# Optimization experiments

Measured on AMD Instinct MI355X. Metric: run time of the kernel, lower is better.

## Reference

```python
import jax, jax.numpy as jnp
import numpy as np

# ---- geometry constants (LinearProbeGeom) ----
N_DET, N_T = 128, 2048
NX, NY = 128, 256
PITCH, DT = 3.0e-4, 2.5e-8
C_SOUND = 1540.0
X0, DX = 0.0, 3.0e-4
Y0, DY = 1.0e-3, 1.5e-4
ARRAY_X0, ARRAY_Y = 0.0, 0.0

_freq = np.fft.rfftfreq(N_T, d=DT).astype(np.float32)
OMEGA = jnp.asarray(2.0 * np.pi * _freq, dtype=jnp.float32)            # [n_f]
KX = jnp.asarray((2.0 * np.pi * np.fft.fftfreq(N_DET, d=PITCH)).astype(np.float32))  # [n_det]
_fw = np.ones(_freq.shape[0], dtype=np.float32)
if _fw.shape[0] > 2:
    _fw[1:-1] = 2.0
if N_T % 2 == 0 and _fw.shape[0] > 1:
    _fw[-1] = 1.0
FREQ_W = jnp.asarray(_fw)                                              # [n_f]
XC = jnp.asarray((X0 + np.arange(NX) * DX - ARRAY_X0).astype(np.float32))  # [nx]
YC = jnp.asarray((Y0 + np.arange(NY) * DY - ARRAY_Y).astype(np.float32))   # [ny]


def setup_inputs() -> dict:
    key = jax.random.key(0)
    sino = jax.random.normal(key, (8, 2, N_DET, N_T), dtype=jnp.float32)
    # Hann window apodization (non-trainable buffer in the torch module)
    win = 0.5 - 0.5 * np.cos(2 * np.pi * np.arange(N_DET) / max(N_DET - 1, 1))
    apod = jnp.asarray(win.astype(np.float32))
    return {"sino": sino, "apod": apod}


def reference(sino, apod):
    B, C, n_det, n_t = sino.shape
    eps = jnp.finfo(jnp.float32).eps
    # per-(B,C) standardization over (n_det, n_t)
    mean = sino.mean(axis=(-2, -1), keepdims=True)
    sn = sino - mean
    std = jnp.sqrt(jnp.mean(sn * sn, axis=(-2, -1), keepdims=True) + eps)
    sn = sn / std
    sw = sn * apod[None, None, :, None]
    # temporal rFFT then spatial FFT over detectors -> [B,C,n_det,n_f] complex64
    spec = jnp.fft.fft(jnp.fft.rfft(sw, axis=-1), axis=2)
    kz_sq = (OMEGA / C_SOUND)[None, :] ** 2 - (KX ** 2)[:, None]       # [n_det,n_f]
    kz = jnp.sqrt(jnp.clip(kz_sq, 0.0))
    spec = spec * (kz_sq > 0).astype(spec.dtype)
    # phase factors (vectorized over all ny depths -> one big contraction)
    phase_x = jnp.exp(1j * KX[:, None] * XC[None, :]).astype(spec.dtype)        # [n_det,nx]
    phase_y = jnp.exp(1j * YC[:, None, None] * kz[None, :, :]).astype(spec.dtype)  # [ny,n_det,n_f]
    specw = spec * FREQ_W.astype(spec.dtype)[None, None, None, :]
    band = jnp.einsum('bcdf,ydf->bcyd', specw, phase_y)                # sum over freq
    img_c = jnp.einsum('bcyd,dx->bcyx', band, phase_x)                 # [B,C,ny,nx]
    img = jnp.abs(img_c).astype(sino.dtype)
    norm = jnp.maximum(apod.sum(), eps) * jnp.maximum(FREQ_W.sum(), eps)
    return img / norm
```

## Files before the change

### kernel.cpp

```cpp
#include <hip/hip_runtime.h>
#include <math.h>

#define N_DETC 128
#define N_TC   2048
#define N_FC   1025
#define N_FP   1056
#define NXC    128
#define NYC    256
#define NBCC   16

#define MPAD(i) ((i) + ((i) >> 5))

typedef short bf16x8 __attribute__((ext_vector_type(8)));
typedef float f32x4  __attribute__((ext_vector_type(4)));

__device__ __forceinline__ float2 cmulf(float2 a, float2 b){
    return make_float2(a.x*b.x - a.y*b.y, a.x*b.y + a.y*b.x);
}

#if __has_builtin(__builtin_amdgcn_sinf) && __has_builtin(__builtin_amdgcn_cosf)
__device__ __forceinline__ float sin_rev(float tf){ return __builtin_amdgcn_sinf(tf); }
__device__ __forceinline__ float cos_rev(float tf){ return __builtin_amdgcn_cosf(tf); }
#else
__device__ __forceinline__ float sin_rev(float tf){ return __sinf(6.28318530718f * tf); }
__device__ __forceinline__ float cos_rev(float tf){ return __cosf(6.28318530718f * tf); }
#endif

__device__ __forceinline__ ushort cvt_bf16(float x){
    uint u = __float_as_uint(x);
    return (ushort)((u + 0x7FFFu + ((u >> 16) & 1u)) >> 16);
}

__global__ __launch_bounds__(256) void k_tfft(const float* __restrict__ sino,
                                              float* __restrict__ psum,
                                              float* __restrict__ psq,
                                              uint* __restrict__ spec_u){
    int row = blockIdx.x;
    __shared__ float2 z[1055];
    __shared__ float ls[4], lq[4];
    int tid = threadIdx.x;
    const float2* p = (const float2*)(sino + (size_t)row * N_TC);
    float s = 0.f, q = 0.f;
    for (int n = tid; n < 1024; n += 256){
        float2 v = p[n];
        s += v.x + v.y;
        q += v.x * v.x + v.y * v.y;
        int r = __brev((unsigned)n) >> 22;
        z[MPAD(r)] = v;
    }
    #pragma unroll
    for (int m = 1; m < 64; m <<= 1){
        s += __shfl_xor(s, m, 64);
        q += __shfl_xor(q, m, 64);
    }
    int w = tid >> 6, lane = tid & 63;
    if (lane == 0){ ls[w] = s; lq[w] = q; }
    __syncthreads();
    if (tid == 0){
        psum[row] = ls[0] + ls[1] + ls[2] + ls[3];
        psq[row]  = lq[0] + lq[1] + lq[2] + lq[3];
    }
    #pragma unroll
    for (int st = 0; st < 5; ++st){
        int h = 1 << (2 * st);
        int qd = tid;
        int k = qd & (h - 1);
        int g = qd >> (2 * st);
        int base = (g << (2 * st + 2)) + k;
        float2 x0 = z[MPAD(base)];
        float2 x1 = z[MPAD(base + h)];
        float2 x2 = z[MPAD(base + 2 * h)];
        float2 x3 = z[MPAD(base + 3 * h)];
        float a1 = -(float)M_PI * (float)k / (float)h;
        float s1, c1; __sincosf(a1, &s1, &c1);
        float a2 = 0.5f * a1;
        float s2, c2; __sincosf(a2, &s2, &c2);
        float2 t1 = make_float2(x1.x * c1 - x1.y * s1, x1.x * s1 + x1.y * c1);
        float2 t3 = make_float2(x3.x * c1 - x3.y * s1, x3.x * s1 + x3.y * c1);
        float2 y0 = make_float2(x0.x + t1.x, x0.y + t1.y);
        float2 y1 = make_float2(x0.x - t1.x, x0.y - t1.y);
        float2 y2 = make_float2(x2.x + t3.x, x2.y + t3.y);
        float2 y3 = make_float2(x2.x - t3.x, x2.y - t3.y);
        float2 u = make_float2(y2.x * c2 - y2.y * s2, y2.x * s2 + y2.y * c2);
        float2 v = make_float2(y3.x * c2 - y3.y * s2, y3.x * s2 + y3.y * c2);
        float2 wv = make_float2(v.y, -v.x);
        z[MPAD(base)]         = make_float2(y0.x + u.x, y0.y + u.y);
        z[MPAD(base + 2 * h)] = make_float2(y0.x - u.x, y0.y - u.y);
        z[MPAD(base + h)]     = make_float2(y1.x + wv.x, y1.y + wv.y);
        z[MPAD(base + 3 * h)] = make_float2(y1.x - wv.x, y1.y - wv.y);
        __syncthreads();
    }
    uint* o = spec_u + (size_t)row * N_FC;
    for (int k = tid; k < 1025; k += 256){
        float2 A  = z[MPAD(k & 1023)];
        float2 Bv = z[MPAD((1024 - k) & 1023)];
        float Br = Bv.x, Bi = -Bv.y;
        float Er = 0.5f * (A.x + Br), Ei = 0.5f * (A.y + Bi);
        float Dr = 0.5f * (A.x - Br), Di = 0.5f * (A.y - Bi);
        float Or = Di, Oi = -Dr;
        float ang = -(float)M_PI * (float)k * (1.0f / 1024.0f);
        float sn, cs; __sincosf(ang, &sn, &cs);
        float Xr = Er + cs * Or - sn * Oi;
        float Xi = Ei + cs * Oi + sn * Or;
        uint pk;
        asm("v_cvt_pk_bf16_f32 %0, %1, %2" : "=v"(pk) : "v"(Xr), "v"(Xi));
        o[k] = pk;
    }
}

__global__ __launch_bounds__(256) void k_dft(const uint* __restrict__ spec_u,
                                             const float* __restrict__ psum,
                                             const float* __restrict__ psq,
                                             const float* __restrict__ apod,
                                             ushort* __restrict__ Arp,
                                             ushort* __restrict__ Aip,
                                             float4* __restrict__ kzJ){
    int bid = blockIdx.x;
    int ft = bid >> 4, bc = bid & 15;
    int f0 = ft << 5;
    int tid = threadIdx.x;
    __shared__ float2 tile[128][33];
    __shared__ ushort stAr[128][40];
    __shared__ ushort stAi[128][40];
    __shared__ float sm[2];

    if (tid < 64){
        float s = psum[bc * 128 + tid] + psum[bc * 128 + 64 + tid];
        float q = psq[bc * 128 + tid] + psq[bc * 128 + 64 + tid];
        #pragma unroll
        for (int m = 1; m < 64; m <<= 1){
            s += __shfl_xor(s, m, 64);
            q += __shfl_xor(q, m, 64);
        }
        if (tid == 0){
            const float inv_n = 1.f / (float)(N_DETC * N_TC);
            float mean = s * inv_n;
            float var  = q * inv_n - mean * mean;
            sm[0] = mean;
            sm[1] = rsqrtf(fmaxf(var, 0.f) + 1.1920929e-7f);
        }
    }
    __syncthreads();
    float mean = sm[0], invstd = sm[1];

    int fl  = tid & 31;
    int kd0 = tid >> 5;
    int f = f0 + fl;
    bool fok = (f <= 1024);
    float fr = (float)f * 19531.25f;
    float oc = fr * (1.0f / 1540.0f);

    #pragma unroll
    for (int i = 0; i < 16; ++i){
        int kd = kd0 + (i << 3);
        int rkd = __brev((unsigned)kd) >> 25;
        uint u = fok ? spec_u[((size_t)(bc * 128 + kd)) * N_FC + f] : 0u;
        float vr = __uint_as_float(u << 16);
        float vi = __uint_as_float(u & 0xFFFF0000u);
        if (f == 0) vr -= mean * 2048.f;
        float sc = apod[kd] * invstd;
        tile[rkd][fl] = make_float2(vr * sc, vi * sc);
    }
    if (bc == 0){
        #pragma unroll
        for (int i = 0; i < 16; ++i){
            int kd = kd0 + (i << 3);
            int sdx = (kd < 64) ? kd : kd - 128;
            float bb = (float)sdx * 26.0416666f;
            float kq = oc * oc - bb * bb;
            float kzr = (fok && kq > 0.f) ? sqrtf(kq) : 0.f;
            float tj = 1.5e-4f * kzr;
            tj -= floorf(tj);
            kzJ[(size_t)kd * N_FP + f] = make_float4(kzr, cos_rev(tj), sin_rev(tj), 0.f);
        }
    }
    __syncthreads();
    #pragma unroll
    for (int st = 0; st < 3; ++st){
        int h = 1 << (2 * st);
        #pragma unroll
        for (int it = 0; it < 4; ++it){
            int task = tid + (it << 8);
            int ff = task & 31;
            int q  = task >> 5;
            int k = q & (h - 1);
            int g = q >> (2 * st);
            int base = (g << (2 * st + 2)) + k;
            float2 x0 = tile[base][ff];
            float2 x1 = tile[base + h][ff];
            float2 x2 = tile[base + 2 * h][ff];
            float2 x3 = tile[base + 3 * h][ff];
            float a1 = -(float)M_PI * (float)k / (float)h;
            float s1, c1; __sincosf(a1, &s1, &c1);
            float a2 = 0.5f * a1;
            float s2, c2; __sincosf(a2, &s2, &c2);
            float2 t1 = make_float2(x1.x * c1 - x1.y * s1, x1.x * s1 + x1.y * c1);
            float2 t3 = make_float2(x3.x * c1 - x3.y * s1, x3.x * s1 + x3.y * c1);
            float2 y0 = make_float2(x0.x + t1.x, x0.y + t1.y);
            float2 y1 = make_float2(x0.x - t1.x, x0.y - t1.y);
            float2 y2 = make_float2(x2.x + t3.x, x2.y + t3.y);
            float2 y3 = make_float2(x2.x - t3.x, x2.y - t3.y);
            float2 u = make_float2(y2.x * c2 - y2.y * s2, y2.x * s2 + y2.y * c2);
            float2 v = make_float2(y3.x * c2 - y3.y * s2, y3.x * s2 + y3.y * c2);
            float2 w = make_float2(v.y, -v.x);
            tile[base][ff]         = make_float2(y0.x + u.x, y0.y + u.y);
            tile[base + 2 * h][ff] = make_float2(y0.x - u.x, y0.y - u.y);
            tile[base + h][ff]     = make_float2(y1.x + w.x, y1.y + w.y);
            tile[base + 3 * h][ff] = make_float2(y1.x - w.x, y1.y - w.y);
        }
        __syncthreads();
    }
    #pragma unroll
    for (int it = 0; it < 8; ++it){
        int task = tid + (it << 8);
        int ff = task & 31, j = task >> 5;
        int i1 = j, i2 = j + 64;
        float ang = -(float)M_PI * (float)j * (1.0f / 64.0f);
        float sn, cs; __sincosf(ang, &sn, &cs);
        float2 u = tile[i1][ff], v = tile[i2][ff];
        float2 t = make_float2(v.x * cs - v.y * sn, v.x * sn + v.y * cs);
        tile[i1][ff] = make_float2(u.x + t.x, u.y + t.y);
        tile[i2][ff] = make_float2(u.x - t.x, u.y - t.y);
    }
    __syncthreads();
    float fw = (f == 0 || f == 1024) ? 1.f : 2.f;
    #pragma unroll
    for (int i = 0; i < 16; ++i){
        int kd = kd0 + (i << 3);
        int sdx = (kd < 64) ? kd : kd - 128;
        float bb = (float)sdx * 26.0416666f;
        float m = (fok && (oc * oc - bb * bb > 0.f)) ? fw : 0.f;
        float2 v = tile[kd][fl];
        stAr[kd][fl] = cvt_bf16(v.x * m);
        stAi[kd][fl] = cvt_bf16(v.y * m);
    }
    __syncthreads();
    int kds = tid >> 1, hf = tid & 1;
    size_t rowoff = ((size_t)kds * 16 + bc) * N_FP + f0 + hf * 16;
    uint4 r0 = *(const uint4*)&stAr[kds][hf * 16];
    uint4 r1 = *(const uint4*)&stAr[kds][hf * 16 + 8];
    uint4 i0 = *(const uint4*)&stAi[kds][hf * 16];
    uint4 i1v = *(const uint4*)&stAi[kds][hf * 16 + 8];
    ((uint4*)(Arp + rowoff))[0] = r0;
    ((uint4*)(Arp + rowoff))[1] = r1;
    ((uint4*)(Aip + rowoff))[0] = i0;
    ((uint4*)(Aip + rowoff))[1] = i1v;
}

__global__ __launch_bounds__(512) void k_band(const ushort* __restrict__ Ar,
                                              const ushort* __restrict__ Ai,
                                              const float4* __restrict__ kzJ,
                                              float2* __restrict__ band_p){
    int blk = blockIdx.x;
    int fc = blk & 1;
    int yh = (blk >> 1) & 1;
    int kd = blk >> 2;
    int nt = fc ? 17 : 16;
    int tid  = threadIdx.x;
    int wid  = tid >> 6;
    int lane = tid & 63;
    int fp = tid & 15;
    int yq = tid >> 4;
    float ymg = 1.0e-3f + 1.5e-4f * (float)(yh * 128 + yq * 4);

    __shared__ ushort Bls[2][2][128][40];

    int arow = lane & 15;
    int koff = (lane >> 4) * 8;
    int ylocal = wid * 16 + arow;
    const ushort* Arp = Ar + ((size_t)kd * 16 + arow) * N_FP + koff + fc * 512;
    const ushort* Aip = Ai + ((size_t)kd * 16 + arow) * N_FP + koff + fc * 512;
    const float4* kjb = kzJ + (size_t)kd * N_FP + fc * 512;

    auto GENC = [&](float4 k0, float4 k1, int buf){
        float t0 = ymg * k0.x; t0 -= floorf(t0);
        float t1 = ymg * k1.x; t1 -= floorf(t1);
        float cA = cos_rev(t0), sA = sin_rev(t0);
        float cB = cos_rev(t1), sB = sin_rev(t1);
        #pragma unroll
        for (int j = 0; j < 4; ++j){
            int y = yq * 4 + j;
            uint br, bi;
            asm("v_cvt_pk_bf16_f32 %0, %1, %2" : "=v"(br) : "v"(cA), "v"(cB));
            asm("v_cvt_pk_bf16_f32 %0, %1, %2" : "=v"(bi) : "v"(sA), "v"(sB));
            *(uint*)&Bls[buf][0][y][fp * 2] = br;
            *(uint*)&Bls[buf][1][y][fp * 2] = bi;
            if (j < 3){
                float nA = fmaf(cA, k0.y, -(sA * k0.z));
                float mA = fmaf(sA, k0.y,  (cA * k0.z));
                cA = nA; sA = mA;
                float nB = fmaf(cB, k1.y, -(sB * k1.z));
                float mB = fmaf(sB, k1.y,  (cB * k1.z));
                cB = nB; sB = mB;
            }
        }
    };

    f32x4 P1 = {0.f,0.f,0.f,0.f}, P2 = P1, P3 = P1, P4 = P1;

    bf16x8 car = *(const bf16x8*)(Arp);
    bf16x8 cai = *(const bf16x8*)(Aip);
    GENC(kjb[fp * 2], kjb[fp * 2 + 1], 0);
    __syncthreads();

    for (int t = 0; t < nt; ++t){
        bf16x8 nar, nai;
        float4 k0, k1;
        if (t < nt - 1){
            nar = *(const bf16x8*)(Arp + (t + 1) * 32);
            nai = *(const bf16x8*)(Aip + (t + 1) * 32);
            k0 = kjb[(t + 1) * 32 + fp * 2];
            k1 = kjb[(t + 1) * 32 + fp * 2 + 1];
        }
        int buf = t & 1;
        bf16x8 br = *(const bf16x8*)&Bls[buf][0][ylocal][koff];
        bf16x8 bi = *(const bf16x8*)&Bls[buf][1][ylocal][koff];
        P1 = __builtin_amdgcn_mfma_f32_16x16x32_bf16(car, br, P1, 0, 0, 0);
        P2 = __builtin_amdgcn_mfma_f32_16x16x32_bf16(cai, bi, P2, 0, 0, 0);
        P3 = __builtin_amdgcn_mfma_f32_16x16x32_bf16(car, bi, P3, 0, 0, 0);
        P4 = __builtin_amdgcn_mfma_f32_16x16x32_bf16(cai, br, P4, 0, 0, 0);
        if (t < nt - 1){
            GENC(k0, k1, buf ^ 1);
        }
        __syncthreads();
        if (t < nt - 1){ car = nar; cai = nai; }
    }

    int y = yh * 128 + wid * 16 + (lane & 15);
    #pragma unroll
    for (int r = 0; r < 4; ++r){
        int bc = (lane >> 4) * 4 + r;
        band_p[(((size_t)fc * 128 + kd) * 16 + bc) * 256 + y] = make_float2(P1[r] - P2[r], P3[r] + P4[r]);
    }
}

__global__ __launch_bounds__(256) void k_final(const float2* __restrict__ band_p,
                                               const float* __restrict__ apod,
                                               float* __restrict__ out){
    int blk = blockIdx.x;
    int bc = blk >> 5, yt = blk & 31;
    __shared__ float2 tile[128][9];
    __shared__ float asum;
    int tid = threadIdx.x;
    if (tid < 64){
        float a = apod[tid] + apod[tid + 64];
        #pragma unroll
        for (int m = 1; m < 64; m <<= 1) a += __shfl_xor(a, m, 64);
        if (tid == 0) asum = a;
    }
    #pragma unroll
    for (int k2 = 0; k2 < 4; ++k2){
        int idx = tid + k2 * 256;
        int kd = idx >> 3, yi = idx & 7;
        size_t o0 = (((size_t)0 * 128 + kd) * 16 + bc) * 256 + yt * 8 + yi;
        size_t o1 = (((size_t)1 * 128 + kd) * 16 + bc) * 256 + yt * 8 + yi;
        float2 a = band_p[o0], b = band_p[o1];
        int rkd = __brev((unsigned)kd) >> 25;
        tile[rkd][yi] = make_float2(a.x + b.x, a.y + b.y);
    }
    __syncthreads();
    #pragma unroll
    for (int st = 0; st < 3; ++st){
        int h = 1 << (2 * st);
        int q  = tid >> 3;
        int yi = tid & 7;
        int k = q & (h - 1);
        int g = q >> (2 * st);
        int base = (g << (2 * st + 2)) + k;
        float2 x0 = tile[base][yi];
        float2 x1 = tile[base + h][yi];
        float2 x2 = tile[base + 2 * h][yi];
        float2 x3 = tile[base + 3 * h][yi];
        float a1 = (float)M_PI * (float)k / (float)h;
        float s1, c1; __sincosf(a1, &s1, &c1);
        float a2 = 0.5f * a1;
        float s2, c2; __sincosf(a2, &s2, &c2);
        float2 t1 = make_float2(x1.x * c1 - x1.y * s1, x1.x * s1 + x1.y * c1);
        float2 t3 = make_float2(x3.x * c1 - x3.y * s1, x3.x * s1 + x3.y * c1);
        float2 y0 = make_float2(x0.x + t1.x, x0.y + t1.y);
        float2 y1 = make_float2(x0.x - t1.x, x0.y - t1.y);
        float2 y2 = make_float2(x2.x + t3.x, x2.y + t3.y);
        float2 y3 = make_float2(x2.x - t3.x, x2.y - t3.y);
        float2 u = make_float2(y2.x * c2 - y2.y * s2, y2.x * s2 + y2.y * c2);
        float2 v = make_float2(y3.x * c2 - y3.y * s2, y3.x * s2 + y3.y * c2);
        float2 w = make_float2(-v.y, v.x);
        tile[base][yi]         = make_float2(y0.x + u.x, y0.y + u.y);
        tile[base + 2 * h][yi] = make_float2(y0.x - u.x, y0.y - u.y);
        tile[base + h][yi]     = make_float2(y1.x + w.x, y1.y + w.y);
        tile[base + 3 * h][yi] = make_float2(y1.x - w.x, y1.y - w.y);
        __syncthreads();
    }
    #pragma unroll
    for (int it = 0; it < 2; ++it){
        int task = tid + (it << 8);
        int yi = task & 7, j = task >> 3;
        float ang = (float)M_PI * (float)j * (1.0f / 64.0f);
        float sn, cs; __sincosf(ang, &sn, &cs);
        float2 u = tile[j][yi], v = tile[j + 64][yi];
        float2 t = make_float2(v.x * cs - v.y * sn, v.x * sn + v.y * cs);
        tile[j][yi]      = make_float2(u.x + t.x, u.y + t.y);
        tile[j + 64][yi] = make_float2(u.x - t.x, u.y - t.y);
    }
    __syncthreads();
    float invnorm = 1.f / (fmaxf(asum, 1.1920929e-7f) * 2048.f);
    #pragma unroll
    for (int k2 = 0; k2 < 4; ++k2){
        int idx = tid + k2 * 256;
        int x = idx & 127, yi = idx >> 7;
        float2 v = tile[x][yi];
        int y = yt * 8 + yi;
        out[((size_t)bc * 256 + y) * 128 + x] = sqrtf(v.x * v.x + v.y * v.y) * invnorm;
    }
}

extern "C" void kernel_launch(void* const* d_in, const int* in_sizes, int n_in,
                              void* d_out, int out_size, void* d_ws, size_t ws_size,
                              hipStream_t stream){
    const float* sino = (const float*)d_in[0];
    const float* apod = (const float*)d_in[1];
    float* out = (float*)d_out;
    float* W = (float*)d_ws;
    float* psum = W;
    float* psq  = W + 2048;
    uint*   spec_u = (uint*)(W + 4096);
    ushort* Arp    = (ushort*)(W + 4096 + 2099200);
    ushort* Aip    = Arp + (size_t)16 * 128 * N_FP;
    float4* kzJ    = (float4*)(W + 4096 + 2099200 + 2162688);
    float2* band_p = (float2*)(W + 4096 + 2099200 + 2162688 + 540672);

    k_tfft  <<<NBCC * N_DETC, 256, 0, stream>>>(sino, psum, psq, spec_u);
    k_dft   <<<33 * 16, 256, 0, stream>>>(spec_u, psum, psq, apod, Arp, Aip, kzJ);
    k_band  <<<512, 512, 0, stream>>>(Arp, Aip, kzJ, band_p);
    k_final <<<NBCC * 32, 256, 0, stream>>>(band_p, apod, out);
}
```

Baseline: 65.47 us.

## Split frequency reduction four ways, store band partials as bf16, drop LDS staging

k_band now splits the frequency sum into four chunks instead of two, doubling the grid to 1024 blocks so the machine holds more work in flight. The partial band results are packed to bf16 pairs to halve partial-sum traffic, and k_final sums four partials. k_dft writes bf16 outputs straight to global memory instead of staging them in LDS for vectorized stores. The scattered 2-byte stores may coalesce worse, and the bf16 partials lose precision in the intermediate sum.

```diff
diff --git a/kernel.cpp b/kernel.cpp
--- a/kernel.cpp
+++ b/kernel.cpp
@@ -120,8 +120,6 @@
     int f0 = ft << 5;
     int tid = threadIdx.x;
     __shared__ float2 tile[128][33];
-    __shared__ ushort stAr[128][40];
-    __shared__ ushort stAi[128][40];
     __shared__ float sm[2];
 
     if (tid < 64){
@@ -231,31 +229,21 @@
         float bb = (float)sdx * 26.0416666f;
         float m = (fok && (oc * oc - bb * bb > 0.f)) ? fw : 0.f;
         float2 v = tile[kd][fl];
-        stAr[kd][fl] = cvt_bf16(v.x * m);
-        stAi[kd][fl] = cvt_bf16(v.y * m);
-    }
-    __syncthreads();
-    int kds = tid >> 1, hf = tid & 1;
-    size_t rowoff = ((size_t)kds * 16 + bc) * N_FP + f0 + hf * 16;
-    uint4 r0 = *(const uint4*)&stAr[kds][hf * 16];
-    uint4 r1 = *(const uint4*)&stAr[kds][hf * 16 + 8];
-    uint4 i0 = *(const uint4*)&stAi[kds][hf * 16];
-    uint4 i1v = *(const uint4*)&stAi[kds][hf * 16 + 8];
-    ((uint4*)(Arp + rowoff))[0] = r0;
-    ((uint4*)(Arp + rowoff))[1] = r1;
-    ((uint4*)(Aip + rowoff))[0] = i0;
-    ((uint4*)(Aip + rowoff))[1] = i1v;
+        size_t o = ((size_t)kd * 16 + bc) * N_FP + f;
+        Arp[o] = cvt_bf16(v.x * m);
+        Aip[o] = cvt_bf16(v.y * m);
+    }
 }
 
 __global__ __launch_bounds__(512) void k_band(const ushort* __restrict__ Ar,
                                               const ushort* __restrict__ Ai,
                                               const float4* __restrict__ kzJ,
-                                              float2* __restrict__ band_p){
+                                              uint* __restrict__ band_u){
     int blk = blockIdx.x;
-    int fc = blk & 1;
-    int yh = (blk >> 1) & 1;
-    int kd = blk >> 2;
-    int nt = fc ? 17 : 16;
+    int fc = blk & 3;
+    int yh = (blk >> 2) & 1;
+    int kd = blk >> 3;
+    int nt = (fc == 3) ? 9 : 8;
     int tid  = threadIdx.x;
     int wid  = tid >> 6;
     int lane = tid & 63;
@@ -268,9 +256,9 @@
     int arow = lane & 15;
     int koff = (lane >> 4) * 8;
     int ylocal = wid * 16 + arow;
-    const ushort* Arp = Ar + ((size_t)kd * 16 + arow) * N_FP + koff + fc * 512;
-    const ushort* Aip = Ai + ((size_t)kd * 16 + arow) * N_FP + koff + fc * 512;
-    const float4* kjb = kzJ + (size_t)kd * N_FP + fc * 512;
+    const ushort* Arp = Ar + ((size_t)kd * 16 + arow) * N_FP + koff + fc * 256;
+    const ushort* Aip = Ai + ((size_t)kd * 16 + arow) * N_FP + koff + fc * 256;
+    const float4* kjb = kzJ + (size_t)kd * N_FP + fc * 256;
 
     auto GENC = [&](float4 k0, float4 k1, int buf){
         float t0 = ymg * k0.x; t0 -= floorf(t0);
@@ -330,11 +318,15 @@
     #pragma unroll
     for (int r = 0; r < 4; ++r){
         int bc = (lane >> 4) * 4 + r;
-        band_p[(((size_t)fc * 128 + kd) * 16 + bc) * 256 + y] = make_float2(P1[r] - P2[r], P3[r] + P4[r]);
-    }
-}
-
-__global__ __launch_bounds__(256) void k_final(const float2* __restrict__ band_p,
+        float cr = P1[r] - P2[r];
+        float ci = P3[r] + P4[r];
+        uint pk;
+        asm("v_cvt_pk_bf16_f32 %0, %1, %2" : "=v"(pk) : "v"(cr), "v"(ci));
+        band_u[(((size_t)fc * 128 + kd) * 16 + bc) * 256 + y] = pk;
+    }
+}
+
+__global__ __launch_bounds__(256) void k_final(const uint* __restrict__ band_u,
                                                const float* __restrict__ apod,
                                                float* __restrict__ out){
     int blk = blockIdx.x;
@@ -352,11 +344,15 @@
     for (int k2 = 0; k2 < 4; ++k2){
         int idx = tid + k2 * 256;
         int kd = idx >> 3, yi = idx & 7;
-        size_t o0 = (((size_t)0 * 128 + kd) * 16 + bc) * 256 + yt * 8 + yi;
-        size_t o1 = (((size_t)1 * 128 + kd) * 16 + bc) * 256 + yt * 8 + yi;
-        float2 a = band_p[o0], b = band_p[o1];
+        float sr = 0.f, si = 0.f;
+        #pragma unroll
+        for (int p = 0; p < 4; ++p){
+            uint u = band_u[(((size_t)p * 128 + kd) * 16 + bc) * 256 + yt * 8 + yi];
+            sr += __uint_as_float(u << 16);
+            si += __uint_as_float(u & 0xFFFF0000u);
+        }
         int rkd = __brev((unsigned)kd) >> 25;
-        tile[rkd][yi] = make_float2(a.x + b.x, a.y + b.y);
+        tile[rkd][yi] = make_float2(sr, si);
     }
     __syncthreads();
     #pragma unroll
@@ -426,10 +422,10 @@
     ushort* Arp    = (ushort*)(W + 4096 + 2099200);
     ushort* Aip    = Arp + (size_t)16 * 128 * N_FP;
     float4* kzJ    = (float4*)(W + 4096 + 2099200 + 2162688);
-    float2* band_p = (float2*)(W + 4096 + 2099200 + 2162688 + 540672);
+    uint*   band_u = (uint*)(W + 4096 + 2099200 + 2162688 + 540672);
 
     k_tfft  <<<NBCC * N_DETC, 256, 0, stream>>>(sino, psum, psq, spec_u);
     k_dft   <<<33 * 16, 256, 0, stream>>>(spec_u, psum, psq, apod, Arp, Aip, kzJ);
-    k_band  <<<512, 512, 0, stream>>>(Arp, Aip, kzJ, band_p);
-    k_final <<<NBCC * 32, 256, 0, stream>>>(band_p, apod, out);
-}
+    k_band  <<<1024, 512, 0, stream>>>(Arp, Aip, kzJ, band_u);
+    k_final <<<NBCC * 32, 256, 0, stream>>>(band_u, apod, out);
+}
```

Result: faster. 61.15 us (-6.6%).
